# Kernel tuning notes

Measured on AMD Instinct MI355X. Metric: run time of the kernel, lower is better.

## Reference

```python
import jax, jax.numpy as jnp
import numpy as np

B, S, E = 8, 2048, 128
DECAY = 1.2
LN_EPS = 1e-3  # keras LayerNormalization default epsilon


def setup_inputs() -> dict:
    key = jax.random.key(0)
    k1, k2, k3, k4 = jax.random.split(key, 4)
    return {
        "x": jax.random.normal(k1, (B, S, E), dtype=jnp.float32),
        "dense_w": jax.random.normal(k2, (E, E), dtype=jnp.float32) * 0.02,
        "dense_b": jnp.zeros((E,), dtype=jnp.float32),
        "concept_map": jax.random.normal(k3, (E, E, E), dtype=jnp.float32) * 0.02,
        "ln_gamma": jnp.ones((E,), dtype=jnp.float32),
        "ln_beta": jnp.zeros((E,), dtype=jnp.float32),
    }


def reference(x, dense_w, dense_b, concept_map, ln_gamma, ln_beta):
    # Dense projection
    h = x @ dense_w + dense_b  # (B, S, E)
    b, s, e = h.shape

    # Decayed prefix-sum recurrence: s_i = (s_{i-1} + h_{i-1}) / 1.2, s_0 = 0
    def step(carry, xt):
        new = (carry + xt) / DECAY
        return new, new

    h_t = jnp.swapaxes(h, 0, 1)  # (S, B, E)
    _, s_tail = jax.lax.scan(step, jnp.zeros((b, e), h.dtype), h_t[:-1])
    s_seq = jnp.concatenate([jnp.zeros((1, b, e), h.dtype), s_tail], axis=0)
    s_seq = jnp.swapaxes(s_seq, 0, 1)  # (B, S, E)

    # result[b,s,c] = sum_{a,p} h[b,s,a] * s_seq[b,s,p] * W[c,a,p]
    # (original code materializes (B,S,E,E,E); this is the fused contraction)
    out = jnp.einsum("bsa,bsp,cap->bsc", h, s_seq, concept_map)

    r = out + h
    # LayerNormalization over the last axis
    mean = jnp.mean(r, axis=-1, keepdims=True)
    var = jnp.var(r, axis=-1, keepdims=True)
    r = (r - mean) * jax.lax.rsqrt(var + LN_EPS) * ln_gamma + ln_beta
    # Dropout is identity at inference
    return r
```

## Files before the change

kernel.cpp:

```cpp
#include <hip/hip_runtime.h>
#include <hip/hip_bf16.h>
#include <math.h>

#define E_DIM 128
#define S_LEN 2048
#define B_N   8
#define BS    (B_N * S_LEN)
#define CHUNK 64
#define NCHUNK (S_LEN / CHUNK)

typedef unsigned short u16;
typedef __attribute__((ext_vector_type(8)))  short s8v;
typedef __attribute__((ext_vector_type(16))) float f32x16;

__global__ __launch_bounds__(256) void k_dense(const float* __restrict__ x,
                                               const float* __restrict__ w,
                                               const float* __restrict__ bias,
                                               float* __restrict__ hout) {
    __shared__ float Wl[E_DIM * E_DIM];
    const int t = threadIdx.x;
    const long r0 = (long)blockIdx.x * 64;

    float4* Wl4 = (float4*)Wl;
    const float4* w4 = (const float4*)w;
#pragma unroll
    for (int i = 0; i < 16; ++i) Wl4[t + 256 * i] = w4[t + 256 * i];
    __syncthreads();

    const int cq = t & 31;
    const int rg = t >> 5;
    float4 bb = ((const float4*)bias)[cq];
    float acc[8][4];
#pragma unroll
    for (int i = 0; i < 8; ++i) {
        acc[i][0] = bb.x; acc[i][1] = bb.y; acc[i][2] = bb.z; acc[i][3] = bb.w;
    }
#pragma unroll 4
    for (int k = 0; k < E_DIM; ++k) {
        float4 wv = Wl4[k * 32 + cq];
#pragma unroll
        for (int i = 0; i < 8; ++i) {
            float xv = x[(r0 + rg * 8 + i) * E_DIM + k];
            acc[i][0] += xv * wv.x;
            acc[i][1] += xv * wv.y;
            acc[i][2] += xv * wv.z;
            acc[i][3] += xv * wv.w;
        }
    }
    float4* h4 = (float4*)(hout + r0 * E_DIM);
#pragma unroll
    for (int i = 0; i < 8; ++i) {
        float4 o;
        o.x = acc[i][0]; o.y = acc[i][1]; o.z = acc[i][2]; o.w = acc[i][3];
        h4[(rg * 8 + i) * 32 + cq] = o;
    }
}

__global__ __launch_bounds__(128) void k_scan(const float* __restrict__ h,
                                              float* __restrict__ sbuf,
                                              float* __restrict__ fc) {
    const int b = blockIdx.x >> 5;
    const int j = blockIdx.x & 31;
    const int e = threadIdx.x;
    const float inv_d = (float)(1.0 / 1.2);
    long base = ((long)(b * S_LEN + j * CHUNK)) * E_DIM + e;
    float carry = 0.f;
#pragma unroll 4
    for (int i = 0; i < CHUNK; ++i) {
        sbuf[base + (long)i * E_DIM] = carry;
        carry = (carry + h[base + (long)i * E_DIM]) * inv_d;
    }
    fc[(b * NCHUNK + j) * E_DIM + e] = carry;
}

__global__ __launch_bounds__(256) void k_carry(float* __restrict__ fc, float dm64) {
    int t = blockIdx.x * 256 + threadIdx.x;
    int b = t >> 7, e = t & 127;
    float c = 0.f;
    for (int j = 0; j < NCHUNK; ++j) {
        int idx = (b * NCHUNK + j) * E_DIM + e;
        float v = fc[idx];
        fc[idx] = c;
        c = v + c * dm64;
    }
}

__global__ __launch_bounds__(256) void k_fix(float* __restrict__ sbuf,
                                             const float* __restrict__ fc) {
    const float L2D = 0.26303440583379383f;
    int idx4 = blockIdx.x * 256 + threadIdx.x;
    int e4   = idx4 & 31;
    int pos  = idx4 >> 5;
    int sidx = pos & (S_LEN - 1);
    int b    = pos >> 11;
    int i    = sidx & (CHUNK - 1);
    int j    = sidx >> 6;
    float f = exp2f(-L2D * (float)i);
    float4 cv = ((const float4*)fc)[(b * NCHUNK + j) * 32 + e4];
    float4 sv = ((float4*)sbuf)[idx4];
    sv.x += cv.x * f; sv.y += cv.y * f; sv.z += cv.z * f; sv.w += cv.w * f;
    ((float4*)sbuf)[idx4] = sv;
}

__global__ __launch_bounds__(256) void k_wconv(const float* __restrict__ cm,
                                               u16* __restrict__ wb) {
    int t = blockIdx.x * 256 + threadIdx.x;
    int qs = t & 15, c = (t >> 4) & 127, a = t >> 11;
    const float* src = cm + (((long)(c << 7) + a) << 7) + ((qs ^ (c & 15)) << 3);
    float4 v0 = ((const float4*)src)[0];
    float4 v1 = ((const float4*)src)[1];
    union { __hip_bfloat162 h2[4]; s8v v; } u;
    u.h2[0] = __float22bfloat162_rn(make_float2(v0.x, v0.y));
    u.h2[1] = __float22bfloat162_rn(make_float2(v0.z, v0.w));
    u.h2[2] = __float22bfloat162_rn(make_float2(v1.x, v1.y));
    u.h2[3] = __float22bfloat162_rn(make_float2(v1.z, v1.w));
    ((s8v*)wb)[t] = u.v;
}

__global__ __launch_bounds__(256, 2) void k_main(const float* __restrict__ h,
                                                 const float* __restrict__ sbuf,
                                                 const u16* __restrict__ wb,
                                                 float* __restrict__ out) {
    __shared__ u16 Wl[2][16384];
    const int t = threadIdx.x;
    const int w = t >> 6;
    const int l = t & 63;
    const int l31 = l & 31, hi = l >> 5;
    const int mb = blockIdx.x >> 1, r = blockIdx.x & 1;
    const long gr = (long)mb * 128 + w * 32 + l31;

    float sreg[64];
    const float4* s4 = (const float4*)(sbuf + gr * E_DIM);
#pragma unroll
    for (int ks = 0; ks < 8; ++ks) {
        float4 v0 = s4[ks * 4 + hi * 2];
        float4 v1 = s4[ks * 4 + hi * 2 + 1];
        sreg[ks*8+0]=v0.x; sreg[ks*8+1]=v0.y; sreg[ks*8+2]=v0.z; sreg[ks*8+3]=v0.w;
        sreg[ks*8+4]=v1.x; sreg[ks*8+5]=v1.y; sreg[ks*8+6]=v1.z; sreg[ks*8+7]=v1.w;
    }

    f32x16 acc[4];
#pragma unroll
    for (int nt = 0; nt < 4; ++nt)
#pragma unroll
        for (int g = 0; g < 16; ++g) acc[nt][g] = 0.f;

    const u16* wbase = wb + (size_t)r * 64 * 16384;
    const int cx = l31 & 15;

#pragma unroll
    for (int i = 0; i < 8; ++i) {
        const u16* g = wbase + (w * 8 + i) * 512 + l * 8;
        __builtin_amdgcn_global_load_lds((const __attribute__((address_space(1))) void*)g,
            (__attribute__((address_space(3))) void*)&Wl[0][(w * 8 + i) * 512], 16, 0, 0);
    }
    float hv = h[gr * E_DIM + r * 64];
    __syncthreads();

#pragma unroll 1
    for (int sl = 0; sl < 64; ++sl) {
        const int cur = sl & 1;
        if (sl < 63) {
#pragma unroll
            for (int i = 0; i < 8; ++i) {
                const u16* g = wbase + (size_t)(sl + 1) * 16384 + (w * 8 + i) * 512 + l * 8;
                __builtin_amdgcn_global_load_lds((const __attribute__((address_space(1))) void*)g,
                    (__attribute__((address_space(3))) void*)&Wl[cur ^ 1][(w * 8 + i) * 512], 16, 0, 0);
            }
        }
        float hvn = (sl < 63) ? h[gr * E_DIM + r * 64 + sl + 1] : 0.f;

        s8v af[8];
#pragma unroll
        for (int ks = 0; ks < 8; ++ks) {
            union { __hip_bfloat162 h2[4]; s8v v; } u;
#pragma unroll
            for (int q = 0; q < 4; ++q)
                u.h2[q] = __float22bfloat162_rn(
                    make_float2(hv * sreg[ks*8 + 2*q], hv * sreg[ks*8 + 2*q + 1]));
            af[ks] = u.v;
        }

#pragma unroll
        for (int ks = 0; ks < 8; ++ks) {
            const int dq = ((ks << 1) + hi) ^ cx;
#pragma unroll
            for (int nt = 0; nt < 4; ++nt) {
                s8v bf = *(const s8v*)&Wl[cur][(nt * 32 + l31) * 128 + dq * 8];
                acc[nt] = __builtin_amdgcn_mfma_f32_32x32x16_bf16(af[ks], bf, acc[nt], 0, 0, 0);
            }
        }
        hv = hvn;
        __syncthreads();
    }

#pragma unroll
    for (int nt = 0; nt < 4; ++nt)
#pragma unroll
        for (int g = 0; g < 16; ++g) {
            int rowl = (g & 3) + 8 * (g >> 2) + 4 * hi;
            unsafeAtomicAdd(&out[((long)mb * 128 + w * 32 + rowl) * E_DIM + nt * 32 + l31],
                            acc[nt][g]);
        }
}

__global__ __launch_bounds__(256) void k_ln(float* __restrict__ out,
                                            const float* __restrict__ h,
                                            const float* __restrict__ gamma,
                                            const float* __restrict__ beta) {
    const int t = threadIdx.x;
    const int l32 = t & 31, rl = t >> 5;
    const long row = (long)blockIdx.x * 8 + rl;
    float4 v  = ((const float4*)out)[row * 32 + l32];
    float4 hv = ((const float4*)h)[row * 32 + l32];
    v.x += hv.x; v.y += hv.y; v.z += hv.z; v.w += hv.w;
    float ls = v.x + v.y + v.z + v.w;
    float lq = v.x * v.x + v.y * v.y + v.z * v.z + v.w * v.w;
#pragma unroll
    for (int m = 1; m < 32; m <<= 1) {
        ls += __shfl_xor(ls, m, 64);
        lq += __shfl_xor(lq, m, 64);
    }
    float mean = ls * (1.f / 128.f);
    float var  = lq * (1.f / 128.f) - mean * mean;
    float inv  = rsqrtf(var + 1e-3f);
    float4 g = ((const float4*)gamma)[l32];
    float4 b = ((const float4*)beta)[l32];
    float4 o;
    o.x = (v.x - mean) * inv * g.x + b.x;
    o.y = (v.y - mean) * inv * g.y + b.y;
    o.z = (v.z - mean) * inv * g.z + b.z;
    o.w = (v.w - mean) * inv * g.w + b.w;
    ((float4*)out)[row * 32 + l32] = o;
}

extern "C" void kernel_launch(void* const* d_in, const int* in_sizes, int n_in,
                              void* d_out, int out_size, void* d_ws, size_t ws_size,
                              hipStream_t stream) {
    const float* x     = (const float*)d_in[0];
    const float* dw    = (const float*)d_in[1];
    const float* db    = (const float*)d_in[2];
    const float* cm    = (const float*)d_in[3];
    const float* gamma = (const float*)d_in[4];
    const float* beta  = (const float*)d_in[5];
    float* outp = (float*)d_out;

    float* ws = (float*)d_ws;
    float* h  = ws;
    float* sb = ws + (size_t)BS * E_DIM;
    float* fc = ws + (size_t)2 * BS * E_DIM;
    u16*   wb = (u16*)(ws + (size_t)2 * BS * E_DIM + B_N * NCHUNK * E_DIM);

    float dm64 = (float)pow(1.2, -64.0);

    hipMemsetAsync(d_out, 0, (size_t)BS * E_DIM * sizeof(float), stream);
    k_wconv<<<dim3(1024), dim3(256), 0, stream>>>(cm, wb);
    k_dense<<<dim3(BS / 64), dim3(256), 0, stream>>>(x, dw, db, h);
    k_scan <<<dim3(B_N * NCHUNK), dim3(128), 0, stream>>>(h, sb, fc);
    k_carry<<<dim3(4), dim3(256), 0, stream>>>(fc, dm64);
    k_fix  <<<dim3((BS * E_DIM / 4) / 256), dim3(256), 0, stream>>>(sb, fc);
    k_main <<<dim3(256), dim3(256), 0, stream>>>(h, sb, wb, outp);
    k_ln   <<<dim3(BS / 8), dim3(256), 0, stream>>>(outp, h, gamma, beta);
}
```

Measured before the change: 131.0 us.

## Switch main contraction to fp16 with packed A-fragment math and wider tiles

Stores the scan state and a transposed copy of h in fp16 and converts the concept map to fp16 instead of bf16. The main kernel now builds A fragments with packed fp16 multiplies and uses fp16 MFMA. It also retiles to 512-thread blocks covering 256 rows with a 4-way split over the a dimension, so each block loads fewer W slices and keeps two row blocks per wave. The aim is to cut per-slice conversion ALU work and W traffic per output row. The costs are fp16 range and precision risk in the h*s products, more atomic adds to the output, and extra writes for the hT transpose.

Result: faster. 128.0 us (-2.3%).

```diff
diff --git a/kernel.cpp b/kernel.cpp
--- a/kernel.cpp
+++ b/kernel.cpp
@@ -10,8 +10,10 @@
 #define NCHUNK (S_LEN / CHUNK)
 
 typedef unsigned short u16;
-typedef __attribute__((ext_vector_type(8)))  short s8v;
-typedef __attribute__((ext_vector_type(16))) float f32x16;
+typedef _Float16 f16;
+typedef _Float16 f16x2 __attribute__((ext_vector_type(2)));
+typedef _Float16 f16x8 __attribute__((ext_vector_type(8)));
+typedef float    f32x16 __attribute__((ext_vector_type(16)));
 
 __global__ __launch_bounds__(256) void k_dense(const float* __restrict__ x,
                                                const float* __restrict__ w,
@@ -57,18 +59,29 @@
 }
 
 __global__ __launch_bounds__(128) void k_scan(const float* __restrict__ h,
-                                              float* __restrict__ sbuf,
-                                              float* __restrict__ fc) {
+                                              u16* __restrict__ sb16,
+                                              float* __restrict__ fc,
+                                              u16* __restrict__ hT) {
     const int b = blockIdx.x >> 5;
     const int j = blockIdx.x & 31;
     const int e = threadIdx.x;
     const float inv_d = (float)(1.0 / 1.2);
-    long base = ((long)(b * S_LEN + j * CHUNK)) * E_DIM + e;
+    const int pos0 = b * S_LEN + j * CHUNK;
+    long base = (long)pos0 * E_DIM + e;
     float carry = 0.f;
-#pragma unroll 4
-    for (int i = 0; i < CHUNK; ++i) {
-        sbuf[base + (long)i * E_DIM] = carry;
-        carry = (carry + h[base + (long)i * E_DIM]) * inv_d;
+    union { u16 u[8]; uint4 v; } hb;
+#pragma unroll 1
+    for (int i0 = 0; i0 < CHUNK; i0 += 8) {
+#pragma unroll
+        for (int k = 0; k < 8; ++k) {
+            float hv = h[base + (long)(i0 + k) * E_DIM];
+            union { f16 f; u16 u; } cu; cu.f = (f16)carry;
+            sb16[base + (long)(i0 + k) * E_DIM] = cu.u;
+            union { f16 f; u16 u; } hu; hu.f = (f16)hv;
+            hb.u[k] = hu.u;
+            carry = (carry + hv) * inv_d;
+        }
+        *(uint4*)&hT[(size_t)e * BS + pos0 + i0] = hb.v;
     }
     fc[(b * NCHUNK + j) * E_DIM + e] = carry;
 }
@@ -85,21 +98,28 @@
     }
 }
 
-__global__ __launch_bounds__(256) void k_fix(float* __restrict__ sbuf,
+__global__ __launch_bounds__(256) void k_fix(u16* __restrict__ sb16,
                                              const float* __restrict__ fc) {
     const float L2D = 0.26303440583379383f;
-    int idx4 = blockIdx.x * 256 + threadIdx.x;
-    int e4   = idx4 & 31;
-    int pos  = idx4 >> 5;
-    int sidx = pos & (S_LEN - 1);
-    int b    = pos >> 11;
-    int i    = sidx & (CHUNK - 1);
-    int j    = sidx >> 6;
+    int u = blockIdx.x * 256 + threadIdx.x;
+    int e8  = u & 15;
+    int pos = u >> 4;
+    int i = pos & (CHUNK - 1);
+    int j = (pos >> 6) & (NCHUNK - 1);
+    int b = pos >> 11;
     float f = exp2f(-L2D * (float)i);
-    float4 cv = ((const float4*)fc)[(b * NCHUNK + j) * 32 + e4];
-    float4 sv = ((float4*)sbuf)[idx4];
-    sv.x += cv.x * f; sv.y += cv.y * f; sv.z += cv.z * f; sv.w += cv.w * f;
-    ((float4*)sbuf)[idx4] = sv;
+    const float4* fp = (const float4*)(fc + ((size_t)(b * NCHUNK + j)) * E_DIM + e8 * 8);
+    float4 c0 = fp[0], c1 = fp[1];
+    float cs[8] = {c0.x, c0.y, c0.z, c0.w, c1.x, c1.y, c1.z, c1.w};
+    uint4* sp = (uint4*)(sb16 + (size_t)pos * E_DIM + e8 * 8);
+    union { uint4 v; u16 u[8]; } su; su.v = *sp;
+#pragma unroll
+    for (int k = 0; k < 8; ++k) {
+        union { f16 f; u16 u; } a; a.u = su.u[k];
+        union { f16 f; u16 u; } o; o.f = (f16)((float)a.f + cs[k] * f);
+        su.u[k] = o.u;
+    }
+    *sp = su.v;
 }
 
 __global__ __launch_bounds__(256) void k_wconv(const float* __restrict__ cm,
@@ -109,99 +129,109 @@
     const float* src = cm + (((long)(c << 7) + a) << 7) + ((qs ^ (c & 15)) << 3);
     float4 v0 = ((const float4*)src)[0];
     float4 v1 = ((const float4*)src)[1];
-    union { __hip_bfloat162 h2[4]; s8v v; } u;
-    u.h2[0] = __float22bfloat162_rn(make_float2(v0.x, v0.y));
-    u.h2[1] = __float22bfloat162_rn(make_float2(v0.z, v0.w));
-    u.h2[2] = __float22bfloat162_rn(make_float2(v1.x, v1.y));
-    u.h2[3] = __float22bfloat162_rn(make_float2(v1.z, v1.w));
-    ((s8v*)wb)[t] = u.v;
-}
-
-__global__ __launch_bounds__(256, 2) void k_main(const float* __restrict__ h,
-                                                 const float* __restrict__ sbuf,
+    union { f16 f[8]; uint4 v; } o;
+    o.f[0] = (f16)v0.x; o.f[1] = (f16)v0.y; o.f[2] = (f16)v0.z; o.f[3] = (f16)v0.w;
+    o.f[4] = (f16)v1.x; o.f[5] = (f16)v1.y; o.f[6] = (f16)v1.z; o.f[7] = (f16)v1.w;
+    ((uint4*)wb)[t] = o.v;
+}
+
+__global__ __launch_bounds__(512, 2) void k_main(const u16* __restrict__ hT,
+                                                 const u16* __restrict__ sb16,
                                                  const u16* __restrict__ wb,
                                                  float* __restrict__ out) {
     __shared__ u16 Wl[2][16384];
     const int t = threadIdx.x;
-    const int w = t >> 6;
-    const int l = t & 63;
+    const int w = t >> 6, l = t & 63;
     const int l31 = l & 31, hi = l >> 5;
-    const int mb = blockIdx.x >> 1, r = blockIdx.x & 1;
-    const long gr = (long)mb * 128 + w * 32 + l31;
-
-    float sreg[64];
-    const float4* s4 = (const float4*)(sbuf + gr * E_DIM);
-#pragma unroll
-    for (int ks = 0; ks < 8; ++ks) {
-        float4 v0 = s4[ks * 4 + hi * 2];
-        float4 v1 = s4[ks * 4 + hi * 2 + 1];
-        sreg[ks*8+0]=v0.x; sreg[ks*8+1]=v0.y; sreg[ks*8+2]=v0.z; sreg[ks*8+3]=v0.w;
-        sreg[ks*8+4]=v1.x; sreg[ks*8+5]=v1.y; sreg[ks*8+6]=v1.z; sreg[ks*8+7]=v1.w;
-    }
-
-    f32x16 acc[4];
-#pragma unroll
-    for (int nt = 0; nt < 4; ++nt)
-#pragma unroll
-        for (int g = 0; g < 16; ++g) acc[nt][g] = 0.f;
-
-    const u16* wbase = wb + (size_t)r * 64 * 16384;
-    const int cx = l31 & 15;
-
-#pragma unroll
-    for (int i = 0; i < 8; ++i) {
-        const u16* g = wbase + (w * 8 + i) * 512 + l * 8;
-        __builtin_amdgcn_global_load_lds((const __attribute__((address_space(1))) void*)g,
-            (__attribute__((address_space(3))) void*)&Wl[0][(w * 8 + i) * 512], 16, 0, 0);
-    }
-    float hv = h[gr * E_DIM + r * 64];
+    const int mb = blockIdx.x >> 2, r = blockIdx.x & 3;
+    const int rbp = w >> 1, ntp = w & 1;
+    const int row0 = mb * 256 + rbp * 64 + l31;
+
+    f16x2 s2[2][32];
+#pragma unroll
+    for (int rb = 0; rb < 2; ++rb) {
+        const uint4* sp = (const uint4*)(sb16 + (size_t)(row0 + 32 * rb) * E_DIM + hi * 8);
+#pragma unroll
+        for (int ks = 0; ks < 8; ++ks) {
+            union { uint4 u; f16x2 h2[4]; } uu;
+            uu.u = sp[ks * 2];
+#pragma unroll
+            for (int q = 0; q < 4; ++q) s2[rb][ks * 4 + q] = uu.h2[q];
+        }
+    }
+
+    f32x16 acc[2][2];
+#pragma unroll
+    for (int rb = 0; rb < 2; ++rb)
+#pragma unroll
+        for (int nt = 0; nt < 2; ++nt)
+#pragma unroll
+            for (int g = 0; g < 16; ++g) acc[rb][nt][g] = 0.f;
+
+    const u16* wbK = wb + (size_t)(r * 32) * 16384;
+    const u16* hTb = hT + (size_t)(r * 32) * BS + mb * 256 + rbp * 64 + l31;
+
+#define STAGE(buf, sl) {                                                          \
+    const u16* gsrc = wbK + (size_t)(sl) * 16384 + t * 8;                         \
+    _Pragma("unroll")                                                             \
+    for (int i = 0; i < 4; ++i)                                                   \
+        __builtin_amdgcn_global_load_lds(                                         \
+            (const __attribute__((address_space(1))) void*)(gsrc + i * 4096),     \
+            (__attribute__((address_space(3))) void*)&Wl[buf][t * 8 + i * 4096],  \
+            16, 0, 0); }
+
+    STAGE(0, 0);
+    u16 h0 = hTb[0], h1 = hTb[32];
     __syncthreads();
 
+    const int sxb = l31 & 15;
+    const int wcbase = (ntp * 64 + l31) * E_DIM;
+
 #pragma unroll 1
-    for (int sl = 0; sl < 64; ++sl) {
+    for (int sl = 0; sl < 32; ++sl) {
         const int cur = sl & 1;
-        if (sl < 63) {
-#pragma unroll
-            for (int i = 0; i < 8; ++i) {
-                const u16* g = wbase + (size_t)(sl + 1) * 16384 + (w * 8 + i) * 512 + l * 8;
-                __builtin_amdgcn_global_load_lds((const __attribute__((address_space(1))) void*)g,
-                    (__attribute__((address_space(3))) void*)&Wl[cur ^ 1][(w * 8 + i) * 512], 16, 0, 0);
+        if (sl < 31) {
+            if (cur) STAGE(0, sl + 1) else STAGE(1, sl + 1);
+        }
+        u16 nh0 = 0, nh1 = 0;
+        if (sl < 31) { nh0 = hTb[(size_t)(sl + 1) * BS]; nh1 = hTb[(size_t)(sl + 1) * BS + 32]; }
+
+        union { u16 u[2]; f16x2 v; } hu0, hu1;
+        hu0.u[0] = h0; hu0.u[1] = h0;
+        hu1.u[0] = h1; hu1.u[1] = h1;
+        const u16* Wc = &Wl[cur][wcbase];
+#pragma unroll
+        for (int ks = 0; ks < 8; ++ks) {
+            const int sx = ((ks << 1) + hi) ^ sxb;
+            f16x8 b0 = *(const f16x8*)(Wc + sx * 8);
+            f16x8 b1 = *(const f16x8*)(Wc + 32 * E_DIM + sx * 8);
+            union { f16x2 h2[4]; f16x8 v; } a0, a1;
+#pragma unroll
+            for (int q = 0; q < 4; ++q) {
+                a0.h2[q] = hu0.v * s2[0][ks * 4 + q];
+                a1.h2[q] = hu1.v * s2[1][ks * 4 + q];
             }
-        }
-        float hvn = (sl < 63) ? h[gr * E_DIM + r * 64 + sl + 1] : 0.f;
-
-        s8v af[8];
-#pragma unroll
-        for (int ks = 0; ks < 8; ++ks) {
-            union { __hip_bfloat162 h2[4]; s8v v; } u;
-#pragma unroll
-            for (int q = 0; q < 4; ++q)
-                u.h2[q] = __float22bfloat162_rn(
-                    make_float2(hv * sreg[ks*8 + 2*q], hv * sreg[ks*8 + 2*q + 1]));
-            af[ks] = u.v;
-        }
-
-#pragma unroll
-        for (int ks = 0; ks < 8; ++ks) {
-            const int dq = ((ks << 1) + hi) ^ cx;
-#pragma unroll
-            for (int nt = 0; nt < 4; ++nt) {
-                s8v bf = *(const s8v*)&Wl[cur][(nt * 32 + l31) * 128 + dq * 8];
-                acc[nt] = __builtin_amdgcn_mfma_f32_32x32x16_bf16(af[ks], bf, acc[nt], 0, 0, 0);
+            acc[0][0] = __builtin_amdgcn_mfma_f32_32x32x16_f16(a0.v, b0, acc[0][0], 0, 0, 0);
+            acc[0][1] = __builtin_amdgcn_mfma_f32_32x32x16_f16(a0.v, b1, acc[0][1], 0, 0, 0);
+            acc[1][0] = __builtin_amdgcn_mfma_f32_32x32x16_f16(a1.v, b0, acc[1][0], 0, 0, 0);
+            acc[1][1] = __builtin_amdgcn_mfma_f32_32x32x16_f16(a1.v, b1, acc[1][1], 0, 0, 0);
+        }
+        h0 = nh0; h1 = nh1;
+        __syncthreads();
+    }
+#undef STAGE
+
+#pragma unroll
+    for (int rb = 0; rb < 2; ++rb)
+#pragma unroll
+        for (int nt = 0; nt < 2; ++nt)
+#pragma unroll
+            for (int g = 0; g < 16; ++g) {
+                int rowl = (g & 3) + 8 * (g >> 2) + 4 * hi;
+                long row = (long)mb * 256 + rbp * 64 + rb * 32 + rowl;
+                int col = ntp * 64 + nt * 32 + l31;
+                unsafeAtomicAdd(&out[row * E_DIM + col], acc[rb][nt][g]);
             }
-        }
-        hv = hvn;
-        __syncthreads();
-    }
-
-#pragma unroll
-    for (int nt = 0; nt < 4; ++nt)
-#pragma unroll
-        for (int g = 0; g < 16; ++g) {
-            int rowl = (g & 3) + 8 * (g >> 2) + 4 * hi;
-            unsafeAtomicAdd(&out[((long)mb * 128 + w * 32 + rowl) * E_DIM + nt * 32 + l31],
-                            acc[nt][g]);
-        }
 }
 
 __global__ __launch_bounds__(256) void k_ln(float* __restrict__ out,
@@ -246,19 +276,21 @@
     float* outp = (float*)d_out;
 
     float* ws = (float*)d_ws;
-    float* h  = ws;
-    float* sb = ws + (size_t)BS * E_DIM;
-    float* fc = ws + (size_t)2 * BS * E_DIM;
-    u16*   wb = (u16*)(ws + (size_t)2 * BS * E_DIM + B_N * NCHUNK * E_DIM);
+    float* h   = ws;
+    float* fc  = ws + (size_t)BS * E_DIM;
+    u16*   wb  = (u16*)(fc + B_N * NCHUNK * E_DIM);
+    u16*   hT  = wb + (size_t)E_DIM * E_DIM * E_DIM / 2;
+    hT = wb + (size_t)2097152;
+    u16*   sb16 = hT + (size_t)BS * E_DIM;
 
     float dm64 = (float)pow(1.2, -64.0);
 
     hipMemsetAsync(d_out, 0, (size_t)BS * E_DIM * sizeof(float), stream);
     k_wconv<<<dim3(1024), dim3(256), 0, stream>>>(cm, wb);
     k_dense<<<dim3(BS / 64), dim3(256), 0, stream>>>(x, dw, db, h);
-    k_scan <<<dim3(B_N * NCHUNK), dim3(128), 0, stream>>>(h, sb, fc);
+    k_scan <<<dim3(B_N * NCHUNK), dim3(128), 0, stream>>>(h, sb16, fc, hT);
     k_carry<<<dim3(4), dim3(256), 0, stream>>>(fc, dm64);
-    k_fix  <<<dim3((BS * E_DIM / 4) / 256), dim3(256), 0, stream>>>(sb, fc);
-    k_main <<<dim3(256), dim3(256), 0, stream>>>(h, sb, wb, outp);
+    k_fix  <<<dim3((BS * E_DIM / 8) / 256), dim3(256), 0, stream>>>(sb16, fc);
+    k_main <<<dim3(256), dim3(512), 0, stream>>>(hT, sb16, wb, outp);
     k_ln   <<<dim3(BS / 8), dim3(256), 0, stream>>>(outp, h, gamma, beta);
 }
```
